# Kernel optimization log

Hardware: AMD Instinct MI355X
Metric: run time of the kernel (lower is better)

Reference implementation:

```python
import jax, jax.numpy as jnp
import numpy as np


def setup_inputs() -> dict:
    key = jax.random.key(0)
    kq, kk, kv = jax.random.split(key, 3)
    B, S, D = 4, 4096, 64
    return {
        "q": jax.random.normal(kq, (B, S, D), dtype=jnp.float32),
        "k": jax.random.normal(kk, (B, S, D), dtype=jnp.float32),
        "v": jax.random.normal(kv, (B, S, D), dtype=jnp.float32),
    }


def reference(q, k, v):
    B, S, D = q.shape
    scale = 1.0 / jnp.sqrt(jnp.asarray(D, dtype=q.dtype))
    # (B, S, S) full score matrix, as in the naive torch implementation
    scores = jnp.einsum("bqd,bkd->bqk", q, k) * scale
    causal_mask = jnp.tril(jnp.ones((S, S), dtype=bool))  # True = keep
    scores = jnp.where(causal_mask, scores, -jnp.inf)
    attn = jax.nn.softmax(scores, axis=-1)
    return jnp.einsum("bqk,bkd->bqd", attn, v)
```

## Files before the change

kernel.cpp:

```cpp
#include <hip/hip_runtime.h>
#include <hip/hip_bf16.h>

typedef __bf16 bf16x8 __attribute__((ext_vector_type(8)));
typedef __bf16 bf16x4 __attribute__((ext_vector_type(4)));
typedef float  floatx4 __attribute__((ext_vector_type(4)));

#define SD 4096
#define DH 64
#define NB 4

__device__ __forceinline__ float exp2fast(float x) { return __builtin_amdgcn_exp2f(x); }

__device__ __forceinline__ unsigned pack_bf16_2(float a, float b) {
    union { __bf16 h[2]; unsigned u; } cvt;
    cvt.h[0] = (__bf16)a; cvt.h[1] = (__bf16)b;
    return cvt.u;
}

__device__ __forceinline__ void block_sync_lds() {
    asm volatile("s_waitcnt lgkmcnt(0)\n\ts_barrier" ::: "memory");
}

__global__ __launch_bounds__(256) void prep_kernel(const float* __restrict__ k,
                                                   const float* __restrict__ v,
                                                   __bf16* __restrict__ kb,
                                                   __bf16* __restrict__ vt) {
    __shared__ __bf16 tile[16][80];
    const int bid = blockIdx.x;
    const int tid = threadIdx.x;
    {
        long off = (long)bid * 1024 + tid * 4;
        float4 f = *(const float4*)(k + off);
        bf16x4 o; o[0]=(__bf16)f.x; o[1]=(__bf16)f.y; o[2]=(__bf16)f.z; o[3]=(__bf16)f.w;
        *(bf16x4*)(kb + off) = o;
    }
    const int b = bid >> 8, kt = (bid >> 2) & 63, dq = bid & 3;
    {
        int key = tid >> 2, ds = (tid & 3) * 4;
        float4 f = *(const float4*)(v + ((long)b * SD + kt * 64 + key) * DH + dq * 16 + ds);
        tile[ds+0][key] = (__bf16)f.x;
        tile[ds+1][key] = (__bf16)f.y;
        tile[ds+2][key] = (__bf16)f.z;
        tile[ds+3][key] = (__bf16)f.w;
    }
    __syncthreads();
    {
        int dloc = tid >> 4, cs = (tid & 15) * 4;
        bf16x4 o;
#pragma unroll
        for (int i = 0; i < 4; ++i) {
            int col = cs + i;
            int key = ((col >> 5) * 2 + ((col >> 2) & 1)) * 16
                    + ((col >> 3) & 3) * 4 + (col & 3);
            o[i] = tile[dloc][key];
        }
        *(bf16x4*)(vt + ((long)b * DH + dq * 16 + dloc) * SD + kt * 64 + cs) = o;
    }
}

__global__ __launch_bounds__(256, 2) void fa_kernel(const float* __restrict__ q,
                                                    const __bf16* __restrict__ kb,
                                                    const __bf16* __restrict__ vt,
                                                    float* __restrict__ opart,
                                                    float* __restrict__ lpart) {
    __shared__ __bf16 smem[2][8192];

    const int tid  = threadIdx.x;
    const int wave = tid >> 6;
    const int lane = tid & 63;
    const int c    = lane & 15;
    const int quad = lane >> 4;
    const int bid   = blockIdx.x;
    const int batch = bid & 3;
    const int pr    = (bid >> 2) & 15;
    const int qr    = bid >> 6;
    const float sc = 0.125f * 1.4426950408889634f;

    const long offB   = (long)batch * SD * DH;
    const long vtoffB = (long)batch * DH * SD;

    const int gk0 = tid, gk1 = tid + 256;
    auto swz = [](int g) { int row = g >> 3, ch = g & 7; return row * 64 + ((ch ^ (row & 7)) << 3); };
    const int wk0 = swz(gk0), wk1 = swz(gk1);
    const int wv0 = 4096 + wk0, wv1 = 4096 + wk1;
    const int sw   = c & 7;
    const int off0 = ((quad ^ sw) << 3);
    const int off1 = (((quad + 4) ^ sw) << 3);
    const int rowc = c * 64;

#pragma unroll 1
    for (int ph = 0; ph < 2; ++ph) {
        const int T = ph ? 31 - pr : pr;
        const int myq = T * 128 + wave * 32;

        bf16x8 qf0A, qf1A, qf0B, qf1B;
#pragma unroll
        for (int h = 0; h < 2; ++h) {
            const float* qp = q + offB + (long)(myq + h*16 + c) * DH + quad * 8;
            float4 f0 = *(const float4*)(qp);
            float4 f1 = *(const float4*)(qp + 4);
            float4 f2 = *(const float4*)(qp + 32);
            float4 f3 = *(const float4*)(qp + 36);
            bf16x8 t0, t1;
            t0[0]=(__bf16)(f0.x*sc); t0[1]=(__bf16)(f0.y*sc); t0[2]=(__bf16)(f0.z*sc); t0[3]=(__bf16)(f0.w*sc);
            t0[4]=(__bf16)(f1.x*sc); t0[5]=(__bf16)(f1.y*sc); t0[6]=(__bf16)(f1.z*sc); t0[7]=(__bf16)(f1.w*sc);
            t1[0]=(__bf16)(f2.x*sc); t1[1]=(__bf16)(f2.y*sc); t1[2]=(__bf16)(f2.z*sc); t1[3]=(__bf16)(f2.w*sc);
            t1[4]=(__bf16)(f3.x*sc); t1[5]=(__bf16)(f3.y*sc); t1[6]=(__bf16)(f3.z*sc); t1[7]=(__bf16)(f3.w*sc);
            if (h == 0) { qf0A = t0; qf1A = t1; } else { qf0B = t0; qf1B = t1; }
        }

        floatx4 oA0 = {0.f,0.f,0.f,0.f}, oA1 = oA0, oA2 = oA0, oA3 = oA0;
        floatx4 oB0 = oA0, oB1 = oA0, oB2 = oA0, oB3 = oA0;
        float lA = 0.0f, lB = 0.0f;

        const int kmax = 2 * T + 1;
        const int n = (kmax >= qr) ? ((kmax - qr) >> 3) + 1 : 0;

        bf16x8 sk0, sk1, sv0, sv1;
        auto stage = [&](int kt, bf16x8& a, bf16x8& b, bf16x8& cc, bf16x8& dd) {
            const __bf16* kg = kb + offB + kt * 4096;
            a  = *(const bf16x8*)(kg + gk0 * 8);
            b  = *(const bf16x8*)(kg + gk1 * 8);
            const __bf16* vg = vt + vtoffB + kt * 64;
            cc = *(const bf16x8*)(vg + (long)(gk0 >> 3) * SD + (gk0 & 7) * 8);
            dd = *(const bf16x8*)(vg + (long)(gk1 >> 3) * SD + (gk1 & 7) * 8);
        };

        if (n > 0) stage(qr, sk0, sk1, sv0, sv1);
        block_sync_lds();

#pragma unroll 1
        for (int j = 0; j < n; ++j) {
            const int kt = qr + 8 * j;
            bf16x8 nk0, nk1, nv0, nv1;
            if (j + 1 < n) stage(kt + 8, nk0, nk1, nv0, nv1);
            __bf16* buf = smem[j & 1];
            *(bf16x8*)(buf + wk0) = sk0;
            *(bf16x8*)(buf + wk1) = sk1;
            *(bf16x8*)(buf + wv0) = sv0;
            *(bf16x8*)(buf + wv1) = sv1;
            sk0 = nk0; sk1 = nk1; sv0 = nv0; sv1 = nv1;
            block_sync_lds();

            const int kbase = kt * 64;
            if (kbase > myq + 31) continue;

            const __bf16* kbuf = buf;
            const __bf16* vbuf = buf + 4096;
            floatx4 saA[4], saB[4];
#pragma unroll
            for (int t = 0; t < 4; ++t) {
                bf16x8 ka  = *(const bf16x8*)(kbuf + t * 1024 + rowc + off0);
                bf16x8 kb2 = *(const bf16x8*)(kbuf + t * 1024 + rowc + off1);
                floatx4 a = {0.f,0.f,0.f,0.f}, b = a;
                a = __builtin_amdgcn_mfma_f32_16x16x32_bf16(ka,  qf0A, a, 0, 0, 0);
                a = __builtin_amdgcn_mfma_f32_16x16x32_bf16(kb2, qf1A, a, 0, 0, 0);
                b = __builtin_amdgcn_mfma_f32_16x16x32_bf16(ka,  qf0B, b, 0, 0, 0);
                b = __builtin_amdgcn_mfma_f32_16x16x32_bf16(kb2, qf1B, b, 0, 0, 0);
                saA[t] = a; saB[t] = b;
            }
            float peA[16], peB[16];
            if (kbase + 63 > myq) {
                const int qrA = myq + c, qrB = myq + 16 + c;
#pragma unroll
                for (int t = 0; t < 4; ++t)
#pragma unroll
                    for (int r = 0; r < 4; ++r) {
                        int key = kbase + t*16 + quad*4 + r;
                        peA[t*4+r] = (key <= qrA) ? exp2fast(saA[t][r]) : 0.0f;
                        peB[t*4+r] = (key <= qrB) ? exp2fast(saB[t][r]) : 0.0f;
                    }
            } else {
#pragma unroll
                for (int t = 0; t < 4; ++t)
#pragma unroll
                    for (int r = 0; r < 4; ++r) {
                        peA[t*4+r] = exp2fast(saA[t][r]);
                        peB[t*4+r] = exp2fast(saB[t][r]);
                    }
            }
            {
                float s8[8], s4v[4];
#pragma unroll
                for (int i = 0; i < 8; ++i) s8[i] = peA[i] + peA[i+8];
#pragma unroll
                for (int i = 0; i < 4; ++i) s4v[i] = s8[i] + s8[i+4];
                lA += (s4v[0] + s4v[2]) + (s4v[1] + s4v[3]);
#pragma unroll
                for (int i = 0; i < 8; ++i) s8[i] = peB[i] + peB[i+8];
#pragma unroll
                for (int i = 0; i < 4; ++i) s4v[i] = s8[i] + s8[i+4];
                lB += (s4v[0] + s4v[2]) + (s4v[1] + s4v[3]);
            }
#pragma unroll
            for (int s = 0; s < 2; ++s) {
                union { unsigned u[4]; bf16x8 f; } bpA, bpB;
#pragma unroll
                for (int jj = 0; jj < 4; ++jj) {
                    bpA.u[jj] = pack_bf16_2(peA[8*s + 2*jj], peA[8*s + 2*jj + 1]);
                    bpB.u[jj] = pack_bf16_2(peB[8*s + 2*jj], peB[8*s + 2*jj + 1]);
                }
                const int offs = s ? off1 : off0;
                bf16x8 v0 = *(const bf16x8*)(vbuf + 0*1024 + rowc + offs);
                bf16x8 v1 = *(const bf16x8*)(vbuf + 1*1024 + rowc + offs);
                bf16x8 v2 = *(const bf16x8*)(vbuf + 2*1024 + rowc + offs);
                bf16x8 v3 = *(const bf16x8*)(vbuf + 3*1024 + rowc + offs);
                oA0 = __builtin_amdgcn_mfma_f32_16x16x32_bf16(v0, bpA.f, oA0, 0, 0, 0);
                oA1 = __builtin_amdgcn_mfma_f32_16x16x32_bf16(v1, bpA.f, oA1, 0, 0, 0);
                oA2 = __builtin_amdgcn_mfma_f32_16x16x32_bf16(v2, bpA.f, oA2, 0, 0, 0);
                oA3 = __builtin_amdgcn_mfma_f32_16x16x32_bf16(v3, bpA.f, oA3, 0, 0, 0);
                oB0 = __builtin_amdgcn_mfma_f32_16x16x32_bf16(v0, bpB.f, oB0, 0, 0, 0);
                oB1 = __builtin_amdgcn_mfma_f32_16x16x32_bf16(v1, bpB.f, oB1, 0, 0, 0);
                oB2 = __builtin_amdgcn_mfma_f32_16x16x32_bf16(v2, bpB.f, oB2, 0, 0, 0);
                oB3 = __builtin_amdgcn_mfma_f32_16x16x32_bf16(v3, bpB.f, oB3, 0, 0, 0);
            }
        }

        lA += __shfl_xor(lA, 16); lA += __shfl_xor(lA, 32);
        lB += __shfl_xor(lB, 16); lB += __shfl_xor(lB, 32);

        float* ob = opart + ((long)qr * NB + batch) * (long)(SD * DH) + (long)myq * DH;
        {
            floatx4 ovA[4] = {oA0, oA1, oA2, oA3};
            floatx4 ovB[4] = {oB0, oB1, oB2, oB3};
#pragma unroll
            for (int dt = 0; dt < 4; ++dt) {
                *(floatx4*)(ob + (c)      * DH + dt*16 + quad*4) = ovA[dt];
                *(floatx4*)(ob + (16 + c) * DH + dt*16 + quad*4) = ovB[dt];
            }
        }
        if (quad == 0) {
            lpart[((long)qr * NB + batch) * SD + myq + c]      = lA;
            lpart[((long)qr * NB + batch) * SD + myq + 16 + c] = lB;
        }
    }
}

__global__ __launch_bounds__(256) void combine_kernel(const float* __restrict__ opart,
                                                      const float* __restrict__ lpart,
                                                      float* __restrict__ out) {
    const long idx = (long)blockIdx.x * 256 + threadIdx.x;
    const long qq  = idx >> 6;
    float num = 0.f, den = 0.f;
#pragma unroll
    for (int qr = 0; qr < 8; ++qr) {
        num += opart[((long)qr << 20) + idx];
        den += lpart[((long)qr << 14) + qq];
    }
    out[idx] = num / den;
}

extern "C" void kernel_launch(void* const* d_in, const int* in_sizes, int n_in,
                              void* d_out, int out_size, void* d_ws, size_t ws_size,
                              hipStream_t stream) {
    const float* q = (const float*)d_in[0];
    const float* k = (const float*)d_in[1];
    const float* v = (const float*)d_in[2];
    float* out = (float*)d_out;
    __bf16* kb  = (__bf16*)d_ws;
    __bf16* vtb = kb + (size_t)NB * SD * DH;
    float*  opart = (float*)((char*)d_ws + (4u << 20));
    float*  lpart = (float*)((char*)d_ws + (36u << 20));
    prep_kernel<<<dim3(1024), dim3(256), 0, stream>>>(k, v, kb, vtb);
    fa_kernel<<<dim3(512), dim3(256), 0, stream>>>(q, kb, vtb, opart, lpart);
    combine_kernel<<<dim3(4096), dim3(256), 0, stream>>>(opart, lpart, out);
}
```

Before: 96.84 us.

## Fuse K bf16 conversion into attention kernel and store bf16 partial outputs

K conversion moves out of the prep kernel and into the attention kernel, which loads fp32 K directly and converts while staging into LDS. This removes one write and one read of the bf16 K copy. The split-K partial outputs are stored as bf16 instead of fp32, which halves their write and combine-read traffic. The combine kernel is vectorised to four elements per thread with a reciprocal multiply. In exchange, the attention kernel reads twice the K bytes per tile, and bf16 partial sums lose precision.

```diff
diff --git a/kernel.cpp b/kernel.cpp
--- a/kernel.cpp
+++ b/kernel.cpp
@@ -21,19 +21,11 @@
     asm volatile("s_waitcnt lgkmcnt(0)\n\ts_barrier" ::: "memory");
 }
 
-__global__ __launch_bounds__(256) void prep_kernel(const float* __restrict__ k,
-                                                   const float* __restrict__ v,
-                                                   __bf16* __restrict__ kb,
+__global__ __launch_bounds__(256) void prep_kernel(const float* __restrict__ v,
                                                    __bf16* __restrict__ vt) {
     __shared__ __bf16 tile[16][80];
     const int bid = blockIdx.x;
     const int tid = threadIdx.x;
-    {
-        long off = (long)bid * 1024 + tid * 4;
-        float4 f = *(const float4*)(k + off);
-        bf16x4 o; o[0]=(__bf16)f.x; o[1]=(__bf16)f.y; o[2]=(__bf16)f.z; o[3]=(__bf16)f.w;
-        *(bf16x4*)(kb + off) = o;
-    }
     const int b = bid >> 8, kt = (bid >> 2) & 63, dq = bid & 3;
     {
         int key = tid >> 2, ds = (tid & 3) * 4;
@@ -59,9 +51,9 @@
 }
 
 __global__ __launch_bounds__(256, 2) void fa_kernel(const float* __restrict__ q,
-                                                    const __bf16* __restrict__ kb,
+                                                    const float* __restrict__ kq,
                                                     const __bf16* __restrict__ vt,
-                                                    float* __restrict__ opart,
+                                                    __bf16* __restrict__ opart,
                                                     float* __restrict__ lpart) {
     __shared__ __bf16 smem[2][8192];
 
@@ -79,10 +71,12 @@
     const long offB   = (long)batch * SD * DH;
     const long vtoffB = (long)batch * DH * SD;
 
+    const int krow = tid >> 2, kdc = (tid & 3) * 16;
+    auto swz = [](int g) { int row = g >> 3, ch = g & 7; return row * 64 + ((ch ^ (row & 7)) << 3); };
+    const int wkA = swz(krow * 8 + (tid & 3) * 2);
+    const int wkB = swz(krow * 8 + (tid & 3) * 2 + 1);
     const int gk0 = tid, gk1 = tid + 256;
-    auto swz = [](int g) { int row = g >> 3, ch = g & 7; return row * 64 + ((ch ^ (row & 7)) << 3); };
-    const int wk0 = swz(gk0), wk1 = swz(gk1);
-    const int wv0 = 4096 + wk0, wv1 = 4096 + wk1;
+    const int wv0 = 4096 + swz(gk0), wv1 = 4096 + swz(gk1);
     const int sw   = c & 7;
     const int off0 = ((quad ^ sw) << 3);
     const int off1 = (((quad + 4) ^ sw) << 3);
@@ -116,30 +110,41 @@
         const int kmax = 2 * T + 1;
         const int n = (kmax >= qr) ? ((kmax - qr) >> 3) + 1 : 0;
 
-        bf16x8 sk0, sk1, sv0, sv1;
-        auto stage = [&](int kt, bf16x8& a, bf16x8& b, bf16x8& cc, bf16x8& dd) {
-            const __bf16* kg = kb + offB + kt * 4096;
-            a  = *(const bf16x8*)(kg + gk0 * 8);
-            b  = *(const bf16x8*)(kg + gk1 * 8);
+        float4 fk0, fk1, fk2, fk3;
+        bf16x8 sv0, sv1;
+        auto stage = [&](int kt, float4& a0, float4& a1, float4& a2, float4& a3,
+                         bf16x8& v0, bf16x8& v1) {
+            const float* kg = kq + offB + (long)(kt * 64 + krow) * DH + kdc;
+            a0 = *(const float4*)(kg);
+            a1 = *(const float4*)(kg + 4);
+            a2 = *(const float4*)(kg + 8);
+            a3 = *(const float4*)(kg + 12);
             const __bf16* vg = vt + vtoffB + kt * 64;
-            cc = *(const bf16x8*)(vg + (long)(gk0 >> 3) * SD + (gk0 & 7) * 8);
-            dd = *(const bf16x8*)(vg + (long)(gk1 >> 3) * SD + (gk1 & 7) * 8);
+            v0 = *(const bf16x8*)(vg + (long)(gk0 >> 3) * SD + (gk0 & 7) * 8);
+            v1 = *(const bf16x8*)(vg + (long)(gk1 >> 3) * SD + (gk1 & 7) * 8);
         };
 
-        if (n > 0) stage(qr, sk0, sk1, sv0, sv1);
+        if (n > 0) stage(qr, fk0, fk1, fk2, fk3, sv0, sv1);
         block_sync_lds();
 
 #pragma unroll 1
         for (int j = 0; j < n; ++j) {
             const int kt = qr + 8 * j;
-            bf16x8 nk0, nk1, nv0, nv1;
-            if (j + 1 < n) stage(kt + 8, nk0, nk1, nv0, nv1);
+            float4 nk0, nk1, nk2, nk3; bf16x8 nv0, nv1;
+            if (j + 1 < n) stage(kt + 8, nk0, nk1, nk2, nk3, nv0, nv1);
             __bf16* buf = smem[j & 1];
-            *(bf16x8*)(buf + wk0) = sk0;
-            *(bf16x8*)(buf + wk1) = sk1;
-            *(bf16x8*)(buf + wv0) = sv0;
-            *(bf16x8*)(buf + wv1) = sv1;
-            sk0 = nk0; sk1 = nk1; sv0 = nv0; sv1 = nv1;
+            {
+                bf16x8 cA, cB;
+                cA[0]=(__bf16)fk0.x; cA[1]=(__bf16)fk0.y; cA[2]=(__bf16)fk0.z; cA[3]=(__bf16)fk0.w;
+                cA[4]=(__bf16)fk1.x; cA[5]=(__bf16)fk1.y; cA[6]=(__bf16)fk1.z; cA[7]=(__bf16)fk1.w;
+                cB[0]=(__bf16)fk2.x; cB[1]=(__bf16)fk2.y; cB[2]=(__bf16)fk2.z; cB[3]=(__bf16)fk2.w;
+                cB[4]=(__bf16)fk3.x; cB[5]=(__bf16)fk3.y; cB[6]=(__bf16)fk3.z; cB[7]=(__bf16)fk3.w;
+                *(bf16x8*)(buf + wkA) = cA;
+                *(bf16x8*)(buf + wkB) = cB;
+                *(bf16x8*)(buf + wv0) = sv0;
+                *(bf16x8*)(buf + wv1) = sv1;
+            }
+            fk0 = nk0; fk1 = nk1; fk2 = nk2; fk3 = nk3; sv0 = nv0; sv1 = nv1;
             block_sync_lds();
 
             const int kbase = kt * 64;
@@ -219,14 +224,19 @@
         lA += __shfl_xor(lA, 16); lA += __shfl_xor(lA, 32);
         lB += __shfl_xor(lB, 16); lB += __shfl_xor(lB, 32);
 
-        float* ob = opart + ((long)qr * NB + batch) * (long)(SD * DH) + (long)myq * DH;
+        __bf16* ob = opart + ((long)qr * NB + batch) * (long)(SD * DH) + (long)myq * DH;
         {
             floatx4 ovA[4] = {oA0, oA1, oA2, oA3};
             floatx4 ovB[4] = {oB0, oB1, oB2, oB3};
 #pragma unroll
             for (int dt = 0; dt < 4; ++dt) {
-                *(floatx4*)(ob + (c)      * DH + dt*16 + quad*4) = ovA[dt];
-                *(floatx4*)(ob + (16 + c) * DH + dt*16 + quad*4) = ovB[dt];
+                uint2 sA, sB;
+                sA.x = pack_bf16_2(ovA[dt][0], ovA[dt][1]);
+                sA.y = pack_bf16_2(ovA[dt][2], ovA[dt][3]);
+                sB.x = pack_bf16_2(ovB[dt][0], ovB[dt][1]);
+                sB.y = pack_bf16_2(ovB[dt][2], ovB[dt][3]);
+                *(uint2*)(ob + (c)      * DH + dt*16 + quad*4) = sA;
+                *(uint2*)(ob + (16 + c) * DH + dt*16 + quad*4) = sB;
             }
         }
         if (quad == 0) {
@@ -236,18 +246,22 @@
     }
 }
 
-__global__ __launch_bounds__(256) void combine_kernel(const float* __restrict__ opart,
+__global__ __launch_bounds__(256) void combine_kernel(const __bf16* __restrict__ opart,
                                                       const float* __restrict__ lpart,
                                                       float* __restrict__ out) {
-    const long idx = (long)blockIdx.x * 256 + threadIdx.x;
-    const long qq  = idx >> 6;
-    float num = 0.f, den = 0.f;
+    const long t    = (long)blockIdx.x * 256 + threadIdx.x;
+    const long base = t * 4;
+    const long qq   = base >> 6;
+    float n0 = 0.f, n1 = 0.f, n2 = 0.f, n3 = 0.f, den = 0.f;
 #pragma unroll
     for (int qr = 0; qr < 8; ++qr) {
-        num += opart[((long)qr << 20) + idx];
+        bf16x4 p = *(const bf16x4*)(opart + ((long)qr << 20) + base);
+        n0 += (float)p[0]; n1 += (float)p[1]; n2 += (float)p[2]; n3 += (float)p[3];
         den += lpart[((long)qr << 14) + qq];
     }
-    out[idx] = num / den;
+    float inv = 1.0f / den;
+    float4 o; o.x = n0 * inv; o.y = n1 * inv; o.z = n2 * inv; o.w = n3 * inv;
+    *(float4*)(out + base) = o;
 }
 
 extern "C" void kernel_launch(void* const* d_in, const int* in_sizes, int n_in,
@@ -257,11 +271,10 @@
     const float* k = (const float*)d_in[1];
     const float* v = (const float*)d_in[2];
     float* out = (float*)d_out;
-    __bf16* kb  = (__bf16*)d_ws;
-    __bf16* vtb = kb + (size_t)NB * SD * DH;
-    float*  opart = (float*)((char*)d_ws + (4u << 20));
-    float*  lpart = (float*)((char*)d_ws + (36u << 20));
-    prep_kernel<<<dim3(1024), dim3(256), 0, stream>>>(k, v, kb, vtb);
-    fa_kernel<<<dim3(512), dim3(256), 0, stream>>>(q, kb, vtb, opart, lpart);
-    combine_kernel<<<dim3(4096), dim3(256), 0, stream>>>(opart, lpart, out);
-}
+    __bf16* vtb   = (__bf16*)d_ws;
+    __bf16* opart = (__bf16*)((char*)d_ws + (4u << 20));
+    float*  lpart = (float*)((char*)d_ws + (20u << 20));
+    prep_kernel<<<dim3(1024), dim3(256), 0, stream>>>(v, vtb);
+    fa_kernel<<<dim3(512), dim3(256), 0, stream>>>(q, k, vtb, opart, lpart);
+    combine_kernel<<<dim3(1024), dim3(256), 0, stream>>>(opart, lpart, out);
+}
```

Result: faster. 93.36 us (-3.6%).
